# Optimization experiments

Hardware: AMD Instinct MI355X
Metric: run time of the kernel (lower is better)

Reference implementation:

```python
import jax, jax.numpy as jnp
import numpy as np

N_NODES = 20000
N_EDGES = 200000
D = 64            # node_encoding
H = 4             # num_heads
GRAPH_LAYERS = 2
FLOW_ITERS = 10


def seg_softmax(logits, seg, n):
    # numerically stable softmax over segments (per-row softmax of sparse matrix)
    m = jax.ops.segment_max(logits, seg, num_segments=n)
    e = jnp.exp(logits - m[seg])
    s = jax.ops.segment_sum(e, seg, num_segments=n)
    return e / s[seg]


def setup_inputs() -> dict:
    key = jax.random.key(0)
    ks = jax.random.split(key, 12)
    sc = 1.0 / np.sqrt(D)
    return {
        "node_embeddings": jax.random.normal(ks[0], (N_NODES, D), jnp.float32),
        "demands": jax.random.normal(ks[1], (N_NODES, 1), jnp.float32),
        "edge_row": jax.random.randint(ks[2], (N_EDGES,), 0, N_NODES, jnp.int32),
        "edge_col": jax.random.randint(ks[3], (N_EDGES,), 0, N_NODES, jnp.int32),
        "W_gat": jax.random.normal(ks[4], (H, D, D), jnp.float32) * sc,
        "a_src": jax.random.normal(ks[5], (H, D), jnp.float32) * sc,
        "a_dst": jax.random.normal(ks[6], (H, D), jnp.float32) * sc,
        "Wx": jax.random.normal(ks[7], (D, 3 * D), jnp.float32) * sc,
        "Wh": jax.random.normal(ks[8], (D, 3 * D), jnp.float32) * sc,
        "b_gru": jnp.zeros((3 * D,), jnp.float32),
        "Wd": jax.random.normal(ks[9], (D + 1, 1), jnp.float32) * sc,
        "bd": jnp.zeros((1,), jnp.float32),
    }


def reference(node_embeddings, demands, edge_row, edge_col,
              W_gat, a_src, a_dst, Wx, Wh, b_gru, Wd, bd):
    n = node_embeddings.shape[0]
    h = node_embeddings

    for _ in range(GRAPH_LAYERS):
        # ---- SparseGAT over adjacency edge list ----
        f = jnp.einsum('nd,hde->hne', h, W_gat)          # [H,N,D] per-head features
        s_src = jnp.einsum('hne,he->hn', f, a_src)       # [H,N]
        s_dst = jnp.einsum('hne,he->hn', f, a_dst)       # [H,N]
        logits = jax.nn.leaky_relu(s_src[:, edge_row] + s_dst[:, edge_col], 0.2)  # [H,E]
        alpha = jax.vmap(lambda l: seg_softmax(l, edge_row, n))(logits)           # [H,E]
        msgs = alpha[:, :, None] * f[:, edge_col, :]                              # [H,E,D]
        agg = jax.vmap(lambda m: jax.ops.segment_sum(m, edge_row, num_segments=n))(msgs)  # [H,N,D]
        gat_out = agg.mean(axis=0)                       # average heads -> [N,D]

        # ---- GRU node update (relu candidate activation), state = h ----
        xg = gat_out @ Wx + b_gru                        # [N,3D]
        z = jax.nn.sigmoid(xg[:, :D] + h @ Wh[:, :D])
        r = jax.nn.sigmoid(xg[:, D:2 * D] + h @ Wh[:, D:2 * D])
        hh = jax.nn.relu(xg[:, 2 * D:] + (r * h) @ Wh[:, 2 * D:])
        h = z * h + (1.0 - z) * hh

    # ---- decoder: linear over concat(encoding, demands) ----
    pred_w = jnp.concatenate([h, demands], axis=1) @ Wd + bd   # [N,1]

    # ---- sparse softmax of (adj * pred_weights) per source row ----
    w = seg_softmax(pred_w[edge_row, 0], edge_row, n)          # [E]

    # ---- iterative sparse MCF flow solve ----
    d_pos = jax.nn.relu(demands[:, 0])                         # source injections

    def step(flow, _):
        inflow = d_pos + jax.ops.segment_sum(flow, edge_col, num_segments=n)
        return w * inflow[edge_row], None

    flow, _ = jax.lax.scan(step, jnp.zeros_like(w), None, length=FLOW_ITERS)
    return flow
```

## Files before the change

kernel.cpp:

```cpp
#include <hip/hip_runtime.h>


#define N_NODES 20000
#define N_EDGES 200000
#define NBLK 128
#define NTHR 512
#define NPB 157
#define CAP 24
#define NQUAD 50000
#define QPB 391
#define OFL_MAX 4096
#define NP1 (N_NODES + 1)
#define SPIN_MAX 65536

__device__ __forceinline__ float ld_coh(const float* p) {
    return __hip_atomic_load(p, __ATOMIC_RELAXED, __HIP_MEMORY_SCOPE_AGENT);
}
__device__ __forceinline__ int ld_coh_i(const int* p) {
    return __hip_atomic_load(p, __ATOMIC_RELAXED, __HIP_MEMORY_SCOPE_AGENT);
}
__device__ __forceinline__ void st_coh(float* p, float v) {
    __hip_atomic_store(p, v, __ATOMIC_RELAXED, __HIP_MEMORY_SCOPE_AGENT);
}
__device__ __forceinline__ void st_coh_i(int* p, int v) {
    __hip_atomic_store(p, v, __ATOMIC_RELAXED, __HIP_MEMORY_SCOPE_AGENT);
}

__device__ __forceinline__ void gbar(int* grp, int ord) {
    __syncthreads();
    if (threadIdx.x == 0) {
        __hip_atomic_fetch_add(&grp[(blockIdx.x & 7) * 32], 1,
                               __ATOMIC_RELAXED, __HIP_MEMORY_SCOPE_AGENT);
        const int target = NBLK * ord;
        for (int t = 0; t < SPIN_MAX; ++t) {
            int s = 0;
            #pragma unroll
            for (int g = 0; g < 8; ++g)
                s += __hip_atomic_load(&grp[g * 32], __ATOMIC_RELAXED,
                                       __HIP_MEMORY_SCOPE_AGENT);
            if (s >= target) break;
            __builtin_amdgcn_s_sleep(1);
        }
    }
    __syncthreads();
}

__global__ __launch_bounds__(NTHR)
void mcf_fused(const float* __restrict__ demands,
               const int* __restrict__ edge_row,
               const int* __restrict__ edge_col,
               float* __restrict__ out,
               int* __restrict__ deg,
               int* __restrict__ fill,
               float* __restrict__ V0,
               float* __restrict__ V1b,
               int* __restrict__ pcsc,
               int* __restrict__ ofl_cnt,
               int* __restrict__ ofl_v,
               int* __restrict__ ofl_row,
               int* __restrict__ grp)
{
    const int tx = threadIdx.x, bx = blockIdx.x;
    int bar = 0;

    __shared__ float part[NTHR];

    const int m = bx * QPB + tx;
    const bool bld = (tx < QPB) && (m < NQUAD);
    int4 r4 = {0, 0, 0, 0};
    if (bld) {
        r4 = ((const int4*)edge_row)[m];
        int4 c4 = ((const int4*)edge_col)[m];
        int rr[4] = {r4.x, r4.y, r4.z, r4.w};
        int cc[4] = {c4.x, c4.y, c4.z, c4.w};
        #pragma unroll
        for (int i = 0; i < 4; ++i) {
            __hip_atomic_fetch_add(&deg[rr[i]], 1, __ATOMIC_RELAXED, __HIP_MEMORY_SCOPE_AGENT);
            int idx = __hip_atomic_fetch_add(&fill[cc[i]], 1,
                                             __ATOMIC_RELAXED, __HIP_MEMORY_SCOPE_AGENT);
            if (idx < CAP) {
                st_coh_i(&pcsc[cc[i] * CAP + idx], rr[i]);
            } else {
                int o = __hip_atomic_fetch_add(ofl_cnt, 1,
                                               __ATOMIC_RELAXED, __HIP_MEMORY_SCOPE_AGENT);
                if (o < OFL_MAX) { st_coh_i(&ofl_v[o], cc[i]); st_coh_i(&ofl_row[o], rr[i]); }
            }
        }
    }
    gbar(grp, ++bar);

    const int g = tx / 3, q = tx - 3 * g;
    const int v = bx * NPB + g;
    const bool active = (g < NPB) && (v < N_NODES);
    float dposv = 0.0f, invd = 0.0f;
    int   cnt = 0, ocnt = 0;
    int   er[8];
    if (active) {
        cnt = min(ld_coh_i(&fill[v]), CAP);
        const int4* pb = (const int4*)&pcsc[v * CAP + q * 8];
        int4 a = pb[0], b = pb[1];
        er[0]=a.x; er[1]=a.y; er[2]=a.z; er[3]=a.w;
        er[4]=b.x; er[5]=b.y; er[6]=b.z; er[7]=b.w;
        if (q == 0) {
            dposv  = fmaxf(demands[v], 0.0f);
            int dv = ld_coh_i(&deg[v]);
            invd   = (dv > 0) ? (1.0f / (float)dv) : 0.0f;
            ocnt   = ld_coh_i(ofl_cnt);
        }
        float p = 0.0f;
        #pragma unroll
        for (int s = 0; s < 8; ++s)
            if (q * 8 + s < cnt)
                p += fmaxf(demands[er[s]], 0.0f)
                   * (1.0f / (float)ld_coh_i(&deg[er[s]]));
        part[tx] = p;
    }
    __syncthreads();
    if (active && q == 0) {
        float acc = dposv + part[tx] + part[tx + 1] + part[tx + 2];
        if (ocnt > 0) {
            for (int o = 0; o < ocnt && o < OFL_MAX; ++o)
                if (ld_coh_i(&ofl_v[o]) == v) {
                    int r = ld_coh_i(&ofl_row[o]);
                    acc += fmaxf(demands[r], 0.0f)
                         * (1.0f / (float)ld_coh_i(&deg[r]));
                }
        }
        st_coh(&V0[v], acc * invd);
    }
    gbar(grp, ++bar);

    #pragma unroll 1
    for (int j = 3; j <= 10; ++j) {
        const float* Vp = (j & 1) ? V0 : V1b;
        float*       Vn = (j & 1) ? V1b : V0;
        if (active) {
            float p = 0.0f;
            #pragma unroll
            for (int s = 0; s < 8; ++s)
                if (q * 8 + s < cnt) p += ld_coh(&Vp[er[s]]);
            part[tx] = p;
        }
        __syncthreads();
        if (active && q == 0) {
            float acc = dposv + part[tx] + part[tx + 1] + part[tx + 2];
            if (ocnt > 0) {
                for (int o = 0; o < ocnt && o < OFL_MAX; ++o)
                    if (ld_coh_i(&ofl_v[o]) == v) acc += ld_coh(&Vp[ld_coh_i(&ofl_row[o])]);
            }
            st_coh(&Vn[v], acc * invd);
        }
        gbar(grp, ++bar);
    }

    if (bld) {
        float4 o4;
        o4.x = ld_coh(&V0[r4.x]);
        o4.y = ld_coh(&V0[r4.y]);
        o4.z = ld_coh(&V0[r4.z]);
        o4.w = ld_coh(&V0[r4.w]);
        ((float4*)out)[m] = o4;
    }
}

extern "C" void kernel_launch(void* const* d_in, const int* in_sizes, int n_in,
                              void* d_out, int out_size, void* d_ws, size_t ws_size,
                              hipStream_t stream) {
    const float* demands  = (const float*)d_in[1];
    const int*   edge_row = (const int*)d_in[2];
    const int*   edge_col = (const int*)d_in[3];
    float*       out      = (float*)d_out;

    char* ws = (char*)d_ws;
    auto take = [&](size_t bytes) {
        void* p = (void*)ws;
        ws += (bytes + 127) & ~size_t(127);
        return p;
    };
    char* zone0 = ws;
    int*   deg     = (int*)  take(N_NODES * 4);
    int*   fill    = (int*)  take(N_NODES * 4);
    float* V0      = (float*)take(NP1 * 4);
    float* V1b     = (float*)take(NP1 * 4);
    int*   ofl_cnt = (int*)  take(4);
    int*   grp     = (int*)  take(8 * 32 * 4);
    size_t zone0_bytes = (size_t)(ws - zone0);
    int*   pcsc    = (int*)  take((size_t)N_NODES * CAP * 4);
    int*   ofl_v   = (int*)  take(OFL_MAX * 4);
    int*   ofl_row = (int*)  take(OFL_MAX * 4);

    hipMemsetAsync(zone0, 0x00, zone0_bytes, stream);
    mcf_fused<<<NBLK, NTHR, 0, stream>>>(demands, edge_row, edge_col, out,
                                         deg, fill, V0, V1b, pcsc,
                                         ofl_cnt, ofl_v, ofl_row, grp);
}
```

Baseline: 121.1 us.

## Use 4 lanes per node with shuffle reduction, more blocks, wider barrier counters

Each node's gather now uses 4 lanes (CAP raised to 32) instead of 3, and the partial sums are combined with wavefront shuffles, which removes the shared-memory array and the intra-block __syncthreads from every flow iteration. The grid grows to 160 blocks with 125 nodes each, and the grid barrier's arrival counters are spread over 32 cache lines instead of 8 to reduce atomic contention. The cost is that every spinning block now polls 32 lines, and the larger CAP uses more workspace.

```diff
diff --git a/kernel.cpp b/kernel.cpp
--- a/kernel.cpp
+++ b/kernel.cpp
@@ -3,15 +3,16 @@
 
 #define N_NODES 20000
 #define N_EDGES 200000
-#define NBLK 128
+#define NBLK 160
 #define NTHR 512
-#define NPB 157
-#define CAP 24
+#define NPB 125
+#define CAP 32
 #define NQUAD 50000
-#define QPB 391
+#define QPB 313
 #define OFL_MAX 4096
 #define NP1 (N_NODES + 1)
 #define SPIN_MAX 65536
+#define NLINE 32
 
 __device__ __forceinline__ float ld_coh(const float* p) {
     return __hip_atomic_load(p, __ATOMIC_RELAXED, __HIP_MEMORY_SCOPE_AGENT);
@@ -29,13 +30,13 @@
 __device__ __forceinline__ void gbar(int* grp, int ord) {
     __syncthreads();
     if (threadIdx.x == 0) {
-        __hip_atomic_fetch_add(&grp[(blockIdx.x & 7) * 32], 1,
+        __hip_atomic_fetch_add(&grp[(blockIdx.x & (NLINE - 1)) * 32], 1,
                                __ATOMIC_RELAXED, __HIP_MEMORY_SCOPE_AGENT);
         const int target = NBLK * ord;
         for (int t = 0; t < SPIN_MAX; ++t) {
             int s = 0;
             #pragma unroll
-            for (int g = 0; g < 8; ++g)
+            for (int g = 0; g < NLINE; ++g)
                 s += __hip_atomic_load(&grp[g * 32], __ATOMIC_RELAXED,
                                        __HIP_MEMORY_SCOPE_AGENT);
             if (s >= target) break;
@@ -63,8 +64,6 @@
     const int tx = threadIdx.x, bx = blockIdx.x;
     int bar = 0;
 
-    __shared__ float part[NTHR];
-
     const int m = bx * QPB + tx;
     const bool bld = (tx < QPB) && (m < NQUAD);
     int4 r4 = {0, 0, 0, 0};
@@ -89,9 +88,9 @@
     }
     gbar(grp, ++bar);
 
-    const int g = tx / 3, q = tx - 3 * g;
+    const int g = tx >> 2, q = tx & 3;
     const int v = bx * NPB + g;
-    const bool active = (g < NPB) && (v < N_NODES);
+    const bool active = (g < NPB);
     float dposv = 0.0f, invd = 0.0f;
     int   cnt = 0, ocnt = 0;
     int   er[8];
@@ -113,20 +112,20 @@
             if (q * 8 + s < cnt)
                 p += fmaxf(demands[er[s]], 0.0f)
                    * (1.0f / (float)ld_coh_i(&deg[er[s]]));
-        part[tx] = p;
-    }
-    __syncthreads();
-    if (active && q == 0) {
-        float acc = dposv + part[tx] + part[tx + 1] + part[tx + 2];
-        if (ocnt > 0) {
-            for (int o = 0; o < ocnt && o < OFL_MAX; ++o)
-                if (ld_coh_i(&ofl_v[o]) == v) {
-                    int r = ld_coh_i(&ofl_row[o]);
-                    acc += fmaxf(demands[r], 0.0f)
-                         * (1.0f / (float)ld_coh_i(&deg[r]));
-                }
+        p += __shfl_xor(p, 1);
+        p += __shfl_xor(p, 2);
+        if (q == 0) {
+            float acc = dposv + p;
+            if (ocnt > 0) {
+                for (int o = 0; o < ocnt && o < OFL_MAX; ++o)
+                    if (ld_coh_i(&ofl_v[o]) == v) {
+                        int r = ld_coh_i(&ofl_row[o]);
+                        acc += fmaxf(demands[r], 0.0f)
+                             * (1.0f / (float)ld_coh_i(&deg[r]));
+                    }
+            }
+            st_coh(&V0[v], acc * invd);
         }
-        st_coh(&V0[v], acc * invd);
     }
     gbar(grp, ++bar);
 
@@ -139,16 +138,17 @@
             #pragma unroll
             for (int s = 0; s < 8; ++s)
                 if (q * 8 + s < cnt) p += ld_coh(&Vp[er[s]]);
-            part[tx] = p;
-        }
-        __syncthreads();
-        if (active && q == 0) {
-            float acc = dposv + part[tx] + part[tx + 1] + part[tx + 2];
-            if (ocnt > 0) {
-                for (int o = 0; o < ocnt && o < OFL_MAX; ++o)
-                    if (ld_coh_i(&ofl_v[o]) == v) acc += ld_coh(&Vp[ld_coh_i(&ofl_row[o])]);
+            p += __shfl_xor(p, 1);
+            p += __shfl_xor(p, 2);
+            if (q == 0) {
+                float acc = dposv + p;
+                if (ocnt > 0) {
+                    for (int o = 0; o < ocnt && o < OFL_MAX; ++o)
+                        if (ld_coh_i(&ofl_v[o]) == v)
+                            acc += ld_coh(&Vp[ld_coh_i(&ofl_row[o])]);
+                }
+                st_coh(&Vn[v], acc * invd);
             }
-            st_coh(&Vn[v], acc * invd);
         }
         gbar(grp, ++bar);
     }
@@ -183,7 +183,7 @@
     float* V0      = (float*)take(NP1 * 4);
     float* V1b     = (float*)take(NP1 * 4);
     int*   ofl_cnt = (int*)  take(4);
-    int*   grp     = (int*)  take(8 * 32 * 4);
+    int*   grp     = (int*)  take(NLINE * 32 * 4);
     size_t zone0_bytes = (size_t)(ws - zone0);
     int*   pcsc    = (int*)  take((size_t)N_NODES * CAP * 4);
     int*   ofl_v   = (int*)  take(OFL_MAX * 4);
```

Result: slower. 130.9 us (+8.1%).
